# Performance work log

Hardware: AMD Instinct MI355X
Metric: run time of the kernel (lower is better)

The kernel has to match this reference:

```python
import jax, jax.numpy as jnp
import numpy as np

B, N, D = 2, 4096, 640      # batch, latent tokens, model dim
H, DH = 8, 80               # heads, head dim (H*DH == D)
CN, CD = 77, 768            # context tokens, context dim (CLIP)
FF = 4 * D                  # GEGLU inner dim = 2560
EPS = 1e-5


def _ln(x, w, b):
    m = jnp.mean(x, axis=-1, keepdims=True)
    v = jnp.mean(jnp.square(x - m), axis=-1, keepdims=True)
    return (x - m) * jax.lax.rsqrt(v + EPS) * w + b


def _attn(xq, xkv, wq, wk, wv, wo, bo):
    b, n, _ = xq.shape
    m = xkv.shape[1]
    q = (xq @ wq).reshape(b, n, H, DH).transpose(0, 2, 1, 3)   # b h n d
    k = (xkv @ wk).reshape(b, m, H, DH).transpose(0, 2, 1, 3)  # b h m d
    v = (xkv @ wv).reshape(b, m, H, DH).transpose(0, 2, 1, 3)
    scores = jnp.einsum('bhid,bhjd->bhij', q, k) * (DH ** -0.5)
    attn = jax.nn.softmax(scores, axis=-1)
    out = jnp.einsum('bhij,bhjd->bhid', attn, v)
    out = out.transpose(0, 2, 1, 3).reshape(b, n, H * DH)
    return out @ wo + bo


def setup_inputs() -> dict:
    key = jax.random.key(0)
    ks = jax.random.split(key, 20)
    s = 0.02
    r = lambda k, sh: (jax.random.normal(k, sh, jnp.float32) * s)
    return {
        'x': jax.random.normal(ks[0], (B, N, D), jnp.float32),
        'context': jax.random.normal(ks[1], (B, CN, CD), jnp.float32),
        'ln1_w': jnp.ones((D,), jnp.float32), 'ln1_b': jnp.zeros((D,), jnp.float32),
        'ln2_w': jnp.ones((D,), jnp.float32), 'ln2_b': jnp.zeros((D,), jnp.float32),
        'ln3_w': jnp.ones((D,), jnp.float32), 'ln3_b': jnp.zeros((D,), jnp.float32),
        'wq1': r(ks[2], (D, D)), 'wk1': r(ks[3], (D, D)), 'wv1': r(ks[4], (D, D)),
        'wo1': r(ks[5], (D, D)), 'bo1': jnp.zeros((D,), jnp.float32),
        'wq2': r(ks[6], (D, D)), 'wk2': r(ks[7], (CD, D)), 'wv2': r(ks[8], (CD, D)),
        'wo2': r(ks[9], (D, D)), 'bo2': jnp.zeros((D,), jnp.float32),
        'w_ff1': r(ks[10], (D, 2 * FF)), 'b_ff1': jnp.zeros((2 * FF,), jnp.float32),
        'w_ff2': r(ks[11], (FF, D)), 'b_ff2': jnp.zeros((D,), jnp.float32),
    }


def reference(x, context,
              ln1_w, ln1_b, ln2_w, ln2_b, ln3_w, ln3_b,
              wq1, wk1, wv1, wo1, bo1,
              wq2, wk2, wv2, wo2, bo2,
              w_ff1, b_ff1, w_ff2, b_ff2):
    # self-attention block
    h = _ln(x, ln1_w, ln1_b)
    x = _attn(h, h, wq1, wk1, wv1, wo1, bo1) + x
    # cross-attention block (k/v from context)
    h = _ln(x, ln2_w, ln2_b)
    x = _attn(h, context, wq2, wk2, wv2, wo2, bo2) + x
    # GEGLU feed-forward
    h = _ln(x, ln3_w, ln3_b)
    proj = h @ w_ff1 + b_ff1
    a, g = jnp.split(proj, 2, axis=-1)
    ff = (a * jax.nn.gelu(g, approximate=False)) @ w_ff2 + b_ff2
    return ff + x
```

## Files before the change

kernel.cpp:

```cpp
#include <hip/hip_runtime.h>
#include <hip/hip_bf16.h>

typedef __hip_bfloat16 bf16;
typedef short s16x8 __attribute__((ext_vector_type(8)));
typedef short s16x4 __attribute__((ext_vector_type(4)));
typedef float f32x4 __attribute__((ext_vector_type(4)));

#define SCALE_DH 0.11180339887498949f
#define QSCALE   0.16129820878f

static __device__ __forceinline__ float b2f(short u) {
  union { float f; unsigned int i; } x;
  x.i = ((unsigned int)(unsigned short)u) << 16;
  return x.f;
}

static __device__ __forceinline__ float tof(float x) { return x; }
static __device__ __forceinline__ float tof(bf16 x) { return __bfloat162float(x); }

static __device__ __forceinline__ void gload16(const bf16* g, bf16* l) {
  __builtin_amdgcn_global_load_lds((__attribute__((address_space(1))) const void*)g,
                                   (__attribute__((address_space(3))) void*)l, 16, 0, 0);
}

struct PrepArgs {
  const float* src[10];
  bf16* dst[10];
  int R[10], C[10], cb[10], base[10];
  int cvtbase;
  const float* ctx;
  bf16* ctxb;
};

__global__ __launch_bounds__(256) void prep_kernel(PrepArgs a) {
  const int bid = blockIdx.x;
  if (bid >= a.cvtbase) {
    const int n = 154 * 768;
    int i = ((bid - a.cvtbase) * 256 + threadIdx.x) * 4;
    if (i + 4 <= n) {
      float4 v = *(const float4*)(a.ctx + i);
      a.ctxb[i + 0] = __float2bfloat16(v.x);
      a.ctxb[i + 1] = __float2bfloat16(v.y);
      a.ctxb[i + 2] = __float2bfloat16(v.z);
      a.ctxb[i + 3] = __float2bfloat16(v.w);
    } else {
      for (int k = i; k < n; ++k) a.ctxb[k] = __float2bfloat16(a.ctx[k]);
    }
    return;
  }
  int jid = 0;
#pragma unroll
  for (int k = 1; k < 10; ++k)
    if (bid >= a.base[k]) jid = k;
  const float* in = a.src[jid];
  bf16* out = a.dst[jid];
  const int R = a.R[jid], C = a.C[jid];
  const int lb = bid - a.base[jid];
  const int cblk = lb % a.cb[jid], rblk = lb / a.cb[jid];
  __shared__ float t[32][33];
  const int tx = threadIdx.x & 31, ty = threadIdx.x >> 5;
  const long r0 = (long)rblk * 32, c0 = (long)cblk * 32;
#pragma unroll
  for (int i = 0; i < 4; ++i)
    t[ty + 8 * i][tx] = in[(r0 + ty + 8 * i) * C + c0 + tx];
  __syncthreads();
#pragma unroll
  for (int i = 0; i < 4; ++i)
    out[(c0 + ty + 8 * i) * R + r0 + tx] = __float2bfloat16(t[tx][ty + 8 * i]);
}

template <typename T>
__global__ __launch_bounds__(256) void ln_kernel(const T* __restrict__ x,
                                                 const float* __restrict__ w,
                                                 const float* __restrict__ b,
                                                 bf16* __restrict__ out) {
  const int wv = threadIdx.x >> 6, l = threadIdx.x & 63;
  const long row = (long)blockIdx.x * 4 + wv;
  const T* xr = x + row * 640;
  float v[10];
  float s = 0.f;
#pragma unroll
  for (int j = 0; j < 10; ++j) { v[j] = tof(xr[l + 64 * j]); s += v[j]; }
#pragma unroll
  for (int o = 32; o > 0; o >>= 1) s += __shfl_xor(s, o);
  const float mean = s * (1.f / 640.f);
  float vs = 0.f;
#pragma unroll
  for (int j = 0; j < 10; ++j) { float d = v[j] - mean; vs += d * d; }
#pragma unroll
  for (int o = 32; o > 0; o >>= 1) vs += __shfl_xor(vs, o);
  const float rstd = rsqrtf(vs * (1.f / 640.f) + 1e-5f);
  bf16* orow = out + row * 640;
#pragma unroll
  for (int j = 0; j < 10; ++j) {
    int d = l + 64 * j;
    orow[d] = __float2bfloat16((v[j] - mean) * rstd * w[d] + b[d]);
  }
}

template <int EPI>
__global__ __launch_bounds__(256) void gemm_kernel(const bf16* __restrict__ A,
                                                   const bf16* __restrict__ Bt,
                                                   const float* __restrict__ bias,
                                                   const float* __restrict__ res,
                                                   void* __restrict__ Cout,
                                                   int M, int K, int ldc) {
  __shared__ bf16 Ash[128 * 64];
  __shared__ bf16 Bsh[128 * 64];
  const int tid = threadIdx.x, w = tid >> 6, l = tid & 63;
  const int m0 = blockIdx.x * 128, n0 = blockIdx.y * 128;
  const int mb = (w >> 1) * 64, nb = (w & 1) * 64;
  const int lo = l & 15, lg = l >> 4, lo7 = l & 7;
  const f32x4 fz = {0.f, 0.f, 0.f, 0.f};
  f32x4 acc[4][4];
#pragma unroll
  for (int i = 0; i < 4; ++i)
#pragma unroll
    for (int j = 0; j < 4; ++j) acc[i][j] = fz;

  const int g = tid;
  const int gr = g >> 3;
  const int gcsw = 8 * ((g & 7) ^ (gr & 7));
  const bf16* pa[4];
  const bf16* pb[4];
  bf16* la[4];
  bf16* lb[4];
#pragma unroll
  for (int s = 0; s < 4; ++s) {
    const int rl = gr + 32 * s;
    int ra = m0 + rl; if (ra >= M) ra = M - 1;
    pa[s] = A + (long)ra * K + gcsw;
    pb[s] = Bt + (long)(n0 + rl) * K + gcsw;
    la[s] = Ash + (g + 256 * s) * 8;
    lb[s] = Bsh + (g + 256 * s) * 8;
  }

  for (int k0 = 0; k0 < K; k0 += 64) {
    __syncthreads();
#pragma unroll
    for (int s = 0; s < 4; ++s) {
      gload16(pa[s], la[s]); pa[s] += 64;
      gload16(pb[s], lb[s]); pb[s] += 64;
    }
    __syncthreads();
#pragma unroll
    for (int kk = 0; kk < 2; ++kk) {
      const int sl = ((kk * 4 + lg) ^ lo7) * 8;
      s16x8 a[4], b[4];
#pragma unroll
      for (int i = 0; i < 4; ++i)
        a[i] = *(const s16x8*)(Ash + (mb + i * 16 + lo) * 64 + sl);
#pragma unroll
      for (int j = 0; j < 4; ++j)
        b[j] = *(const s16x8*)(Bsh + (nb + j * 16 + lo) * 64 + sl);
#pragma unroll
      for (int i = 0; i < 4; ++i)
#pragma unroll
        for (int j = 0; j < 4; ++j)
          acc[i][j] = __builtin_amdgcn_mfma_f32_16x16x32_bf16(a[i], b[j], acc[i][j], 0, 0, 0);
    }
  }
  const int rb = m0 + mb + lg * 4;
  const int cb = n0 + nb + lo;
#pragma unroll
  for (int i = 0; i < 4; ++i) {
#pragma unroll
    for (int j = 0; j < 4; ++j) {
      const int col = cb + j * 16;
      if (EPI == 3 && col >= 1280) {
        const int t = col - 1280;
        const int hh = t / 80, dh = t % 80;
        const int row0 = rb + i * 16;
        const int bb = row0 >> 12, n = row0 & 4095;
        s16x4 pk;
#pragma unroll
        for (int r = 0; r < 4; ++r)
          pk[r] = (short)__bfloat16_as_ushort(__float2bfloat16(acc[i][j][r]));
        bf16* vt = (bf16*)res;
        *(s16x4*)(vt + (long)(bb * 8 + hh) * 327680 + (long)dh * 4096 + n) = pk;
        continue;
      }
#pragma unroll
      for (int r = 0; r < 4; ++r) {
        const int row = rb + i * 16 + r;
        if (row < M)
          ((bf16*)Cout)[(long)row * ldc + col] = __float2bfloat16(acc[i][j][r]);
      }
    }
  }
}

template <int EPI>
__global__ __launch_bounds__(256) void gemm64_kernel(const bf16* __restrict__ A,
                                                     const bf16* __restrict__ Bt,
                                                     const float* __restrict__ bias,
                                                     const void* __restrict__ res,
                                                     void* __restrict__ Cout,
                                                     int K, int ldc) {
  __shared__ bf16 Ash[64 * 64];
  __shared__ bf16 Bsh[128 * 64];
  const int tid = threadIdx.x, w = tid >> 6, l = tid & 63;
  const int m0 = blockIdx.x * 64, n0 = blockIdx.y * 128;
  const int mb = (w & 1) * 32, nb = (w >> 1) * 64;
  const int lo = l & 15, lg = l >> 4, lo7 = l & 7;
  const f32x4 fz = {0.f, 0.f, 0.f, 0.f};
  f32x4 acc[2][4];
#pragma unroll
  for (int i = 0; i < 2; ++i)
#pragma unroll
    for (int j = 0; j < 4; ++j) acc[i][j] = fz;

  const int g = tid;
  const int gr = g >> 3;
  const int gcsw = 8 * ((g & 7) ^ (gr & 7));
  const bf16* pa[2];
  const bf16* pb[4];
  bf16* la[2];
  bf16* lb[4];
#pragma unroll
  for (int s = 0; s < 2; ++s) {
    pa[s] = A + (long)(m0 + gr + 32 * s) * K + gcsw;
    la[s] = Ash + (g + 256 * s) * 8;
  }
#pragma unroll
  for (int s = 0; s < 4; ++s) {
    pb[s] = Bt + (long)(n0 + gr + 32 * s) * K + gcsw;
    lb[s] = Bsh + (g + 256 * s) * 8;
  }

  for (int k0 = 0; k0 < K; k0 += 64) {
    __syncthreads();
#pragma unroll
    for (int s = 0; s < 2; ++s) { gload16(pa[s], la[s]); pa[s] += 64; }
#pragma unroll
    for (int s = 0; s < 4; ++s) { gload16(pb[s], lb[s]); pb[s] += 64; }
    __syncthreads();
#pragma unroll
    for (int kk = 0; kk < 2; ++kk) {
      const int sl = ((kk * 4 + lg) ^ lo7) * 8;
      s16x8 a[2], b[4];
#pragma unroll
      for (int i = 0; i < 2; ++i)
        a[i] = *(const s16x8*)(Ash + (mb + i * 16 + lo) * 64 + sl);
#pragma unroll
      for (int j = 0; j < 4; ++j)
        b[j] = *(const s16x8*)(Bsh + (nb + j * 16 + lo) * 64 + sl);
#pragma unroll
      for (int i = 0; i < 2; ++i)
#pragma unroll
        for (int j = 0; j < 4; ++j)
          acc[i][j] = __builtin_amdgcn_mfma_f32_16x16x32_bf16(a[i], b[j], acc[i][j], 0, 0, 0);
    }
  }
  const int rb = m0 + mb + lg * 4;
  const int cb = n0 + nb + lo;
#pragma unroll
  for (int i = 0; i < 2; ++i) {
#pragma unroll
    for (int j = 0; j < 4; ++j) {
      const int col = cb + j * 16;
      float bv = 0.f;
      if (EPI >= 4) bv = bias[col];
#pragma unroll
      for (int r = 0; r < 4; ++r) {
        const int row = rb + i * 16 + r;
        const long idx = (long)row * ldc + col;
        float v = acc[i][j][r] + bv;
        if (EPI == 4) {
          v += ((const float*)res)[idx];
          ((bf16*)Cout)[idx] = __float2bfloat16(v);
        } else if (EPI == 5) {
          v += __bfloat162float(((const bf16*)res)[idx]);
          ((bf16*)Cout)[idx] = __float2bfloat16(v);
        } else if (EPI == 6) {
          v += __bfloat162float(((const bf16*)res)[idx]);
          ((float*)Cout)[idx] = v;
        } else {
          ((bf16*)Cout)[idx] = __float2bfloat16(v);
        }
      }
    }
  }
}

__global__ __launch_bounds__(256, 3) void flash_kernel(const bf16* __restrict__ qkv,
                                                       const bf16* __restrict__ vT,
                                                       bf16* __restrict__ out) {
  __shared__ bf16 Ksh[64 * 80];
  __shared__ bf16 Vsh[80 * 64];
  const int bh = blockIdx.y, b = bh >> 3, h = bh & 7;
  const int tid = threadIdx.x, w = tid >> 6, l = tid & 63;
  const int r0 = blockIdx.x * 128 + w * 32;
  const int lg = l >> 4, lo = l & 15, lo7 = l & 7;
  const int sb = l & 48;
  const s16x8 sz = {0, 0, 0, 0, 0, 0, 0, 0};
  const f32x4 fz = {0.f, 0.f, 0.f, 0.f};

  s16x8 qa[2][3];
#pragma unroll
  for (int gq = 0; gq < 2; ++gq) {
    const bf16* qp = qkv + (long)(b * 4096 + r0 + gq * 16 + lo) * 1920 + h * 80;
    qa[gq][0] = *(const s16x8*)(qp + lg * 8);
    qa[gq][1] = *(const s16x8*)(qp + 32 + lg * 8);
    qa[gq][2] = (lg < 2) ? *(const s16x8*)(qp + 64 + lg * 8) : sz;
#pragma unroll
    for (int f = 0; f < 3; ++f) {
      s16x8 q = qa[gq][f], r;
#pragma unroll
      for (int i = 0; i < 8; ++i)
        r[i] = (short)(__bfloat16_as_ushort(__float2bfloat16(b2f(q[i]) * QSCALE)));
      qa[gq][f] = r;
    }
  }

  const bf16* kp[3];
  const int nbatch = (w < 2) ? 3 : 2;
#pragma unroll
  for (int it = 0; it < 3; ++it) {
    int g = tid + 256 * it;
    int gc = (g < 640) ? g : 0;
    int krow = gc / 10, ksl = gc % 10;
    int ksrc = (ksl < 8) ? (ksl ^ (krow & 7)) : (8 + ((ksl - 8) ^ ((krow >> 2) & 1)));
    kp[it] = qkv + (long)(b * 4096 + krow) * 1920 + 640 + h * 80 + ksrc * 8;
  }
  const bf16* vp0 = vT + (long)bh * 327680 + (long)(tid >> 3) * 4096 +
                    (((tid & 7) ^ ((tid >> 3) & 7)) * 8);
  const int soff0 = tid * 8;

  const int voff0 = (((lg >> 1) + 0) ^ lo7) * 8 + 4 * (lg & 1);
  const int voff1 = (((lg >> 1) + 2) ^ lo7) * 8 + 4 * (lg & 1);
  const int voff2 = (((lg >> 1) + 4) ^ lo7) * 8 + 4 * (lg & 1);
  const int voff3 = (((lg >> 1) + 6) ^ lo7) * 8 + 4 * (lg & 1);

  float lrA = 0.f, lrB = 0.f;
  f32x4 oA[5], oB[5];
#pragma unroll
  for (int dt = 0; dt < 5; ++dt) { oA[dt] = fz; oB[dt] = fz; }

#pragma unroll
  for (int it = 0; it < 3; ++it) {
    if (it < nbatch) {
      gload16(kp[it], Ksh + soff0 + 2048 * it); kp[it] += 64 * 1920;
      gload16(vp0 + (long)it * 131072, Vsh + soff0 + 2048 * it);
    }
  }
  __syncthreads();

  for (int kt = 0; kt < 64; ++kt) {
    unsigned paA[8], paB[8];
    f32x4 s0A, s0B, s1A, s1B;
    {
      s16x8 kb0 = *(const s16x8*)(Ksh + lo * 80 + ((lg ^ lo7)) * 8);
      s16x8 kb1 = *(const s16x8*)(Ksh + lo * 80 + (((4 + lg) ^ lo7)) * 8);
      s16x8 kb2 = (lg < 2) ? *(const s16x8*)(Ksh + lo * 80 + 64 + ((lg ^ ((lo >> 2) & 1))) * 8) : sz;
      __builtin_amdgcn_s_setprio(1);
      s0A = __builtin_amdgcn_mfma_f32_16x16x32_bf16(kb0, qa[0][0], fz, 0, 0, 0);
      s0A = __builtin_amdgcn_mfma_f32_16x16x32_bf16(kb1, qa[0][1], s0A, 0, 0, 0);
      s0A = __builtin_amdgcn_mfma_f32_16x16x32_bf16(kb2, qa[0][2], s0A, 0, 0, 0);
      s0B = __builtin_amdgcn_mfma_f32_16x16x32_bf16(kb0, qa[1][0], fz, 0, 0, 0);
      s0B = __builtin_amdgcn_mfma_f32_16x16x32_bf16(kb1, qa[1][1], s0B, 0, 0, 0);
      s0B = __builtin_amdgcn_mfma_f32_16x16x32_bf16(kb2, qa[1][2], s0B, 0, 0, 0);
      __builtin_amdgcn_s_setprio(0);
    }
#pragma unroll
    for (int ntl = 1; ntl <= 4; ++ntl) {
      if (ntl < 4) {
        s16x8 kb0 = *(const s16x8*)(Ksh + (ntl * 16 + lo) * 80 + ((lg ^ lo7)) * 8);
        s16x8 kb1 = *(const s16x8*)(Ksh + (ntl * 16 + lo) * 80 + (((4 + lg) ^ lo7)) * 8);
        s16x8 kb2 = (lg < 2)
                        ? *(const s16x8*)(Ksh + (ntl * 16 + lo) * 80 + 64 + ((lg ^ ((lo >> 2) & 1))) * 8)
                        : sz;
        __builtin_amdgcn_s_setprio(1);
        s1A = __builtin_amdgcn_mfma_f32_16x16x32_bf16(kb0, qa[0][0], fz, 0, 0, 0);
        s1A = __builtin_amdgcn_mfma_f32_16x16x32_bf16(kb1, qa[0][1], s1A, 0, 0, 0);
        s1A = __builtin_amdgcn_mfma_f32_16x16x32_bf16(kb2, qa[0][2], s1A, 0, 0, 0);
        s1B = __builtin_amdgcn_mfma_f32_16x16x32_bf16(kb0, qa[1][0], fz, 0, 0, 0);
        s1B = __builtin_amdgcn_mfma_f32_16x16x32_bf16(kb1, qa[1][1], s1B, 0, 0, 0);
        s1B = __builtin_amdgcn_mfma_f32_16x16x32_bf16(kb2, qa[1][2], s1B, 0, 0, 0);
        __builtin_amdgcn_s_setprio(0);
      }
      {
        const int pidx = ntl - 1;
        float a0 = __builtin_amdgcn_exp2f(s0A[0]);
        float a1 = __builtin_amdgcn_exp2f(s0A[1]);
        float a2 = __builtin_amdgcn_exp2f(s0A[2]);
        float a3 = __builtin_amdgcn_exp2f(s0A[3]);
        lrA += (a0 + a1) + (a2 + a3);
        unsigned u0, u1;
        asm("v_cvt_pk_bf16_f32 %0, %1, %2" : "=v"(u0) : "v"(a0), "v"(a1));
        asm("v_cvt_pk_bf16_f32 %0, %1, %2" : "=v"(u1) : "v"(a2), "v"(a3));
        paA[pidx * 2] = u0;
        paA[pidx * 2 + 1] = u1;
        float b0 = __builtin_amdgcn_exp2f(s0B[0]);
        float b1 = __builtin_amdgcn_exp2f(s0B[1]);
        float b2 = __builtin_amdgcn_exp2f(s0B[2]);
        float b3 = __builtin_amdgcn_exp2f(s0B[3]);
        lrB += (b0 + b1) + (b2 + b3);
        asm("v_cvt_pk_bf16_f32 %0, %1, %2" : "=v"(u0) : "v"(b0), "v"(b1));
        asm("v_cvt_pk_bf16_f32 %0, %1, %2" : "=v"(u1) : "v"(b2), "v"(b3));
        paB[pidx * 2] = u0;
        paB[pidx * 2 + 1] = u1;
      }
      s0A = s1A;
      s0B = s1B;
    }

    typedef unsigned u32x2 __attribute__((ext_vector_type(2)));
    s16x8 frA0, frA1, frB0, frB1;
    {
      u32x2* p;
      p = (u32x2*)&frA0; p[0] = (u32x2){paA[0], paA[1]}; p[1] = (u32x2){paA[2], paA[3]};
      p = (u32x2*)&frA1; p[0] = (u32x2){paA[4], paA[5]}; p[1] = (u32x2){paA[6], paA[7]};
      p = (u32x2*)&frB0; p[0] = (u32x2){paB[0], paB[1]}; p[1] = (u32x2){paB[2], paB[3]};
      p = (u32x2*)&frB1; p[0] = (u32x2){paB[4], paB[5]}; p[1] = (u32x2){paB[6], paB[7]};
    }

    __syncthreads();

    if (kt < 63) {
#pragma unroll
      for (int it = 0; it < 3; ++it) {
        if (it < nbatch) { gload16(kp[it], Ksh + soff0 + 2048 * it); kp[it] += 64 * 1920; }
      }
    }

    __builtin_amdgcn_s_setprio(1);
#pragma unroll
    for (int dt = 0; dt < 5; ++dt) {
      const bf16* vrow = Vsh + (dt * 16 + lo) * 64;
      s16x4 w00 = *(const s16x4*)(vrow + voff0);
      s16x4 w01 = *(const s16x4*)(vrow + voff1);
      s16x4 w10 = *(const s16x4*)(vrow + voff2);
      s16x4 w11 = *(const s16x4*)(vrow + voff3);
      s16x8 vb0 = __builtin_shufflevector(w00, w01, 0, 1, 2, 3, 4, 5, 6, 7);
      s16x8 vb1 = __builtin_shufflevector(w10, w11, 0, 1, 2, 3, 4, 5, 6, 7);
      oA[dt] = __builtin_amdgcn_mfma_f32_16x16x32_bf16(frA0, vb0, oA[dt], 0, 0, 0);
      oA[dt] = __builtin_amdgcn_mfma_f32_16x16x32_bf16(frA1, vb1, oA[dt], 0, 0, 0);
      oB[dt] = __builtin_amdgcn_mfma_f32_16x16x32_bf16(frB0, vb0, oB[dt], 0, 0, 0);
      oB[dt] = __builtin_amdgcn_mfma_f32_16x16x32_bf16(frB1, vb1, oB[dt], 0, 0, 0);
    }
    __builtin_amdgcn_s_setprio(0);

    __syncthreads();

    if (kt < 63) {
#pragma unroll
      for (int it = 0; it < 3; ++it) {
        if (it < nbatch) gload16(vp0 + (long)(kt + 1) * 64 + (long)it * 131072,
                                 Vsh + soff0 + 2048 * it);
      }
    }
  }

  {
    float ssum = lrA;
    ssum += __shfl_xor(ssum, 16);
    ssum += __shfl_xor(ssum, 32);
    const float linv = 1.f / ssum;
    float li[4];
#pragma unroll
    for (int r = 0; r < 4; ++r) li[r] = __shfl(linv, sb + lg * 4 + r);
    bf16* ob = out + (long)(b * 4096 + r0 + lg * 4) * 640 + h * 80 + lo;
#pragma unroll
    for (int r = 0; r < 4; ++r)
#pragma unroll
      for (int dt = 0; dt < 5; ++dt)
        ob[(long)r * 640 + dt * 16] = __float2bfloat16(oA[dt][r] * li[r]);
  }
  {
    float ssum = lrB;
    ssum += __shfl_xor(ssum, 16);
    ssum += __shfl_xor(ssum, 32);
    const float linv = 1.f / ssum;
    float li[4];
#pragma unroll
    for (int r = 0; r < 4; ++r) li[r] = __shfl(linv, sb + lg * 4 + r);
    bf16* ob = out + (long)(b * 4096 + r0 + 16 + lg * 4) * 640 + h * 80 + lo;
#pragma unroll
    for (int r = 0; r < 4; ++r)
#pragma unroll
      for (int dt = 0; dt < 5; ++dt)
        ob[(long)r * 640 + dt * 16] = __float2bfloat16(oB[dt][r] * li[r]);
  }
}

__global__ __launch_bounds__(256) void cross_kernel(const bf16* __restrict__ q2,
                                                    const bf16* __restrict__ kv2,
                                                    bf16* __restrict__ out) {
  __shared__ bf16 Ksh2[80 * 88];
  __shared__ bf16 Vsh2[80 * 88];
  const int bh = blockIdx.y, b = bh >> 3, h = bh & 7;
  const int tid = threadIdx.x, w = tid >> 6, l = tid & 63;
  const int r0 = blockIdx.x * 128 + w * 32;
  const int lg = l >> 4, lo = l & 15;
  const int sb = l & 48;
  const s16x8 sz = {0, 0, 0, 0, 0, 0, 0, 0};
  const f32x4 fz = {0.f, 0.f, 0.f, 0.f};

  s16x8 qa[2][3];
#pragma unroll
  for (int gq = 0; gq < 2; ++gq) {
    const bf16* qp = q2 + (long)(b * 4096 + r0 + gq * 16 + lo) * 640 + h * 80;
    qa[gq][0] = *(const s16x8*)(qp + lg * 8);
    qa[gq][1] = *(const s16x8*)(qp + 32 + lg * 8);
    qa[gq][2] = (lg < 2) ? *(const s16x8*)(qp + 64 + lg * 8) : sz;
#pragma unroll
    for (int f = 0; f < 3; ++f) {
      s16x8 q = qa[gq][f], r;
#pragma unroll
      for (int i = 0; i < 8; ++i)
        r[i] = (short)(__bfloat16_as_ushort(__float2bfloat16(b2f(q[i]) * QSCALE)));
      qa[gq][f] = r;
    }
  }

  for (int c = tid; c < 800; c += 256) {
    int row = c / 10, s = c % 10;
    s16x8 v = sz;
    if (row < 77)
      v = *(const s16x8*)(kv2 + (long)(b * 77 + row) * 1280 + h * 80 + s * 8);
    *(s16x8*)(Ksh2 + row * 88 + s * 8) = v;
  }
  for (int c = tid; c < 770; c += 256) {
    int j = c / 10, d8 = (c % 10) * 8;
    s16x8 v = *(const s16x8*)(kv2 + (long)(b * 77 + j) * 1280 + 640 + h * 80 + d8);
    const short* vs = (const short*)&v;
#pragma unroll
    for (int i = 0; i < 8; ++i) ((short*)Vsh2)[(d8 + i) * 88 + j] = vs[i];
  }
  if (tid < 240) {
    int d = tid / 3, j = 77 + tid % 3;
    ((short*)Vsh2)[d * 88 + j] = 0;
  }
  __syncthreads();

  float lrA = 0.f, lrB = 0.f;
  f32x4 oA[5], oB[5];
#pragma unroll
  for (int dt = 0; dt < 5; ++dt) { oA[dt] = fz; oB[dt] = fz; }

  unsigned paA[10], paB[10];
  f32x4 s0A, s0B, s1A, s1B;
  {
    s16x8 kb0 = *(const s16x8*)(Ksh2 + lo * 88 + lg * 8);
    s16x8 kb1 = *(const s16x8*)(Ksh2 + lo * 88 + 32 + lg * 8);
    s16x8 kb2 = (lg < 2) ? *(const s16x8*)(Ksh2 + lo * 88 + 64 + lg * 8) : sz;
    __builtin_amdgcn_s_setprio(1);
    s0A = __builtin_amdgcn_mfma_f32_16x16x32_bf16(kb0, qa[0][0], fz, 0, 0, 0);
    s0A = __builtin_amdgcn_mfma_f32_16x16x32_bf16(kb1, qa[0][1], s0A, 0, 0, 0);
    s0A = __builtin_amdgcn_mfma_f32_16x16x32_bf16(kb2, qa[0][2], s0A, 0, 0, 0);
    s0B = __builtin_amdgcn_mfma_f32_16x16x32_bf16(kb0, qa[1][0], fz, 0, 0, 0);
    s0B = __builtin_amdgcn_mfma_f32_16x16x32_bf16(kb1, qa[1][1], s0B, 0, 0, 0);
    s0B = __builtin_amdgcn_mfma_f32_16x16x32_bf16(kb2, qa[1][2], s0B, 0, 0, 0);
    __builtin_amdgcn_s_setprio(0);
  }
#pragma unroll
  for (int ntl = 1; ntl <= 5; ++ntl) {
    if (ntl < 5) {
      s16x8 kb0 = *(const s16x8*)(Ksh2 + (ntl * 16 + lo) * 88 + lg * 8);
      s16x8 kb1 = *(const s16x8*)(Ksh2 + (ntl * 16 + lo) * 88 + 32 + lg * 8);
      s16x8 kb2 = (lg < 2) ? *(const s16x8*)(Ksh2 + (ntl * 16 + lo) * 88 + 64 + lg * 8) : sz;
      __builtin_amdgcn_s_setprio(1);
      s1A = __builtin_amdgcn_mfma_f32_16x16x32_bf16(kb0, qa[0][0], fz, 0, 0, 0);
      s1A = __builtin_amdgcn_mfma_f32_16x16x32_bf16(kb1, qa[0][1], s1A, 0, 0, 0);
      s1A = __builtin_amdgcn_mfma_f32_16x16x32_bf16(kb2, qa[0][2], s1A, 0, 0, 0);
      s1B = __builtin_amdgcn_mfma_f32_16x16x32_bf16(kb0, qa[1][0], fz, 0, 0, 0);
      s1B = __builtin_amdgcn_mfma_f32_16x16x32_bf16(kb1, qa[1][1], s1B, 0, 0, 0);
      s1B = __builtin_amdgcn_mfma_f32_16x16x32_bf16(kb2, qa[1][2], s1B, 0, 0, 0);
      __builtin_amdgcn_s_setprio(0);
    }
    {
      const int pidx = ntl - 1;
      float a0 = __builtin_amdgcn_exp2f(s0A[0]);
      float a1 = __builtin_amdgcn_exp2f(s0A[1]);
      float a2 = __builtin_amdgcn_exp2f(s0A[2]);
      float a3 = __builtin_amdgcn_exp2f(s0A[3]);
      float b0 = __builtin_amdgcn_exp2f(s0B[0]);
      float b1 = __builtin_amdgcn_exp2f(s0B[1]);
      float b2 = __builtin_amdgcn_exp2f(s0B[2]);
      float b3 = __builtin_amdgcn_exp2f(s0B[3]);
      if (pidx == 4) {
        if (lg * 4 + 1 >= 13) { a1 = 0.f; b1 = 0.f; }
        if (lg * 4 + 2 >= 13) { a2 = 0.f; b2 = 0.f; }
        if (lg * 4 + 3 >= 13) { a3 = 0.f; b3 = 0.f; }
      }
      lrA += (a0 + a1) + (a2 + a3);
      lrB += (b0 + b1) + (b2 + b3);
      unsigned u0, u1;
      asm("v_cvt_pk_bf16_f32 %0, %1, %2" : "=v"(u0) : "v"(a0), "v"(a1));
      asm("v_cvt_pk_bf16_f32 %0, %1, %2" : "=v"(u1) : "v"(a2), "v"(a3));
      paA[pidx * 2] = u0;
      paA[pidx * 2 + 1] = u1;
      asm("v_cvt_pk_bf16_f32 %0, %1, %2" : "=v"(u0) : "v"(b0), "v"(b1));
      asm("v_cvt_pk_bf16_f32 %0, %1, %2" : "=v"(u1) : "v"(b2), "v"(b3));
      paB[pidx * 2] = u0;
      paB[pidx * 2 + 1] = u1;
    }
    s0A = s1A;
    s0B = s1B;
  }

  typedef unsigned u32x2 __attribute__((ext_vector_type(2)));
  s16x8 frA0, frA1, frA2, frB0, frB1, frB2;
  {
    u32x2* p;
    p = (u32x2*)&frA0; p[0] = (u32x2){paA[0], paA[1]}; p[1] = (u32x2){paA[2], paA[3]};
    p = (u32x2*)&frA1; p[0] = (u32x2){paA[4], paA[5]}; p[1] = (u32x2){paA[6], paA[7]};
    p = (u32x2*)&frA2; p[0] = (u32x2){paA[8], paA[9]}; p[1] = (u32x2){0u, 0u};
    p = (u32x2*)&frB0; p[0] = (u32x2){paB[0], paB[1]}; p[1] = (u32x2){paB[2], paB[3]};
    p = (u32x2*)&frB1; p[0] = (u32x2){paB[4], paB[5]}; p[1] = (u32x2){paB[6], paB[7]};
    p = (u32x2*)&frB2; p[0] = (u32x2){paB[8], paB[9]}; p[1] = (u32x2){0u, 0u};
  }

  __builtin_amdgcn_s_setprio(1);
#pragma unroll
  for (int dt = 0; dt < 5; ++dt) {
    const bf16* vrow = Vsh2 + (dt * 16 + lo) * 88;
    s16x4 w00 = *(const s16x4*)(vrow + 4 * lg);
    s16x4 w01 = *(const s16x4*)(vrow + 16 + 4 * lg);
    s16x4 w10 = *(const s16x4*)(vrow + 32 + 4 * lg);
    s16x4 w11 = *(const s16x4*)(vrow + 48 + 4 * lg);
    s16x4 w20 = *(const s16x4*)(vrow + 64 + 4 * lg);
    s16x8 vb0 = __builtin_shufflevector(w00, w01, 0, 1, 2, 3, 4, 5, 6, 7);
    s16x8 vb1 = __builtin_shufflevector(w10, w11, 0, 1, 2, 3, 4, 5, 6, 7);
    s16x8 vb2 = __builtin_shufflevector(w20, w20, 0, 1, 2, 3, 0, 1, 2, 3);
    oA[dt] = __builtin_amdgcn_mfma_f32_16x16x32_bf16(frA0, vb0, oA[dt], 0, 0, 0);
    oA[dt] = __builtin_amdgcn_mfma_f32_16x16x32_bf16(frA1, vb1, oA[dt], 0, 0, 0);
    oA[dt] = __builtin_amdgcn_mfma_f32_16x16x32_bf16(frA2, vb2, oA[dt], 0, 0, 0);
    oB[dt] = __builtin_amdgcn_mfma_f32_16x16x32_bf16(frB0, vb0, oB[dt], 0, 0, 0);
    oB[dt] = __builtin_amdgcn_mfma_f32_16x16x32_bf16(frB1, vb1, oB[dt], 0, 0, 0);
    oB[dt] = __builtin_amdgcn_mfma_f32_16x16x32_bf16(frB2, vb2, oB[dt], 0, 0, 0);
  }
  __builtin_amdgcn_s_setprio(0);

  {
    float ssum = lrA;
    ssum += __shfl_xor(ssum, 16);
    ssum += __shfl_xor(ssum, 32);
    const float linv = 1.f / ssum;
    float li[4];
#pragma unroll
    for (int r = 0; r < 4; ++r) li[r] = __shfl(linv, sb + lg * 4 + r);
    bf16* ob = out + (long)(b * 4096 + r0 + lg * 4) * 640 + h * 80 + lo;
#pragma unroll
    for (int r = 0; r < 4; ++r)
#pragma unroll
      for (int dt = 0; dt < 5; ++dt)
        ob[(long)r * 640 + dt * 16] = __float2bfloat16(oA[dt][r] * li[r]);
  }
  {
    float ssum = lrB;
    ssum += __shfl_xor(ssum, 16);
    ssum += __shfl_xor(ssum, 32);
    const float linv = 1.f / ssum;
    float li[4];
#pragma unroll
    for (int r = 0; r < 4; ++r) li[r] = __shfl(linv, sb + lg * 4 + r);
    bf16* ob = out + (long)(b * 4096 + r0 + 16 + lg * 4) * 640 + h * 80 + lo;
#pragma unroll
    for (int r = 0; r < 4; ++r)
#pragma unroll
      for (int dt = 0; dt < 5; ++dt)
        ob[(long)r * 640 + dt * 16] = __float2bfloat16(oB[dt][r] * li[r]);
  }
}

__global__ __launch_bounds__(256) void geglu_kernel(const bf16* __restrict__ A,
                                                    const bf16* __restrict__ Bt,
                                                    const float* __restrict__ bias,
                                                    bf16* __restrict__ Cout) {
  __shared__ bf16 Ash[128 * 64];
  __shared__ bf16 Bsh[2][64 * 64];
  const int tid = threadIdx.x, w = tid >> 6, l = tid & 63;
  const int m0 = blockIdx.x * 128, n0 = blockIdx.y * 64;
  const int lo = l & 15, lg = l >> 4, lo7 = l & 7;
  const int mb = w * 32;
  const f32x4 fz = {0.f, 0.f, 0.f, 0.f};
  f32x4 accA[2][4], accG[2][4];
#pragma unroll
  for (int i = 0; i < 2; ++i)
#pragma unroll
    for (int j = 0; j < 4; ++j) { accA[i][j] = fz; accG[i][j] = fz; }

  const int g = tid;
  const int gr = g >> 3;
  const int gcsw = 8 * ((g & 7) ^ (gr & 7));
  const bf16* pa[4];
  const bf16* pb[2][2];
  bf16* la[4];
  bf16* lb[2][2];
#pragma unroll
  for (int s = 0; s < 4; ++s) {
    pa[s] = A + (long)(m0 + gr + 32 * s) * 640 + gcsw;
    la[s] = Ash + (g + 256 * s) * 8;
  }
#pragma unroll
  for (int q = 0; q < 2; ++q)
#pragma unroll
    for (int s = 0; s < 2; ++s) {
      pb[q][s] = Bt + (long)(n0 + q * 2560 + gr + 32 * s) * 640 + gcsw;
      lb[q][s] = Bsh[q] + (g + 256 * s) * 8;
    }

  for (int k0 = 0; k0 < 640; k0 += 64) {
    __syncthreads();
#pragma unroll
    for (int s = 0; s < 4; ++s) { gload16(pa[s], la[s]); pa[s] += 64; }
#pragma unroll
    for (int q = 0; q < 2; ++q)
#pragma unroll
      for (int s = 0; s < 2; ++s) { gload16(pb[q][s], lb[q][s]); pb[q][s] += 64; }
    __syncthreads();
#pragma unroll
    for (int kk = 0; kk < 2; ++kk) {
      const int sl = ((kk * 4 + lg) ^ lo7) * 8;
      s16x8 a[2], ba[4], bg[4];
#pragma unroll
      for (int i = 0; i < 2; ++i)
        a[i] = *(const s16x8*)(Ash + (mb + i * 16 + lo) * 64 + sl);
#pragma unroll
      for (int j = 0; j < 4; ++j) {
        ba[j] = *(const s16x8*)(Bsh[0] + (j * 16 + lo) * 64 + sl);
        bg[j] = *(const s16x8*)(Bsh[1] + (j * 16 + lo) * 64 + sl);
      }
#pragma unroll
      for (int i = 0; i < 2; ++i)
#pragma unroll
        for (int j = 0; j < 4; ++j) {
          accA[i][j] = __builtin_amdgcn_mfma_f32_16x16x32_bf16(a[i], ba[j], accA[i][j], 0, 0, 0);
          accG[i][j] = __builtin_amdgcn_mfma_f32_16x16x32_bf16(a[i], bg[j], accG[i][j], 0, 0, 0);
        }
    }
  }
#pragma unroll
  for (int i = 0; i < 2; ++i) {
#pragma unroll
    for (int j = 0; j < 4; ++j) {
      const int col = n0 + j * 16 + lo;
      const float bA = bias[col];
      const float bG = bias[2560 + col];
#pragma unroll
      for (int r = 0; r < 4; ++r) {
        const long row = m0 + mb + i * 16 + lg * 4 + r;
        const float av = accA[i][j][r] + bA;
        const float gv = accG[i][j][r] + bG;
        const float ge = 0.5f * gv * (1.f + erff(gv * 0.70710678118654752f));
        Cout[row * 2560 + col] = __float2bfloat16(av * ge);
      }
    }
  }
}

extern "C" void kernel_launch(void* const* d_in, const int* in_sizes, int n_in,
                              void* d_out, int out_size, void* d_ws, size_t ws_size,
                              hipStream_t stream) {
  (void)in_sizes; (void)n_in; (void)out_size; (void)ws_size;
  const float* x    = (const float*)d_in[0];
  const float* ctx  = (const float*)d_in[1];
  const float* ln1w = (const float*)d_in[2];
  const float* ln1b = (const float*)d_in[3];
  const float* ln2w = (const float*)d_in[4];
  const float* ln2b = (const float*)d_in[5];
  const float* ln3w = (const float*)d_in[6];
  const float* ln3b = (const float*)d_in[7];
  const float* wq1  = (const float*)d_in[8];
  const float* wk1  = (const float*)d_in[9];
  const float* wv1  = (const float*)d_in[10];
  const float* wo1  = (const float*)d_in[11];
  const float* bo1  = (const float*)d_in[12];
  const float* wq2  = (const float*)d_in[13];
  const float* wk2  = (const float*)d_in[14];
  const float* wv2  = (const float*)d_in[15];
  const float* wo2  = (const float*)d_in[16];
  const float* bo2  = (const float*)d_in[17];
  const float* wff1 = (const float*)d_in[18];
  const float* bff1 = (const float*)d_in[19];
  const float* wff2 = (const float*)d_in[20];
  const float* bff2 = (const float*)d_in[21];

  char* ws = (char*)d_ws;
  bf16* Wqkv1 = (bf16*)(ws + 0);
  bf16* Wo1t  = (bf16*)(ws + 2457600);
  bf16* Wq2t  = (bf16*)(ws + 3276800);
  bf16* Wkv2t = (bf16*)(ws + 4096000);
  bf16* Wo2t  = (bf16*)(ws + 6062080);
  bf16* Wff1t = (bf16*)(ws + 6881280);
  bf16* Wff2t = (bf16*)(ws + 13434880);
  bf16* Ctxb  = (bf16*)(ws + 16711680);
  bf16* Hln   = (bf16*)(ws + 16948224);
  bf16* X2b   = (bf16*)(ws + 27433984);
  bf16* X3b   = (bf16*)(ws + 48405504);
  bf16* Qkv   = (bf16*)(ws + 69377024);
  bf16* Ffin  = Qkv;
  bf16* Vt    = (bf16*)(ws + 100834304);
  bf16* Ao    = (bf16*)(ws + 111320064);
  bf16* Q2    = (bf16*)(ws + 121805824);
  bf16* Kv2   = (bf16*)(ws + 132291584);
  float* Outf = (float*)d_out;

  dim3 blk(256);

  PrepArgs pa;
  const float* srcs[10] = {wq1, wk1, wv1, wo1, wq2, wk2, wv2, wo2, wff1, wff2};
  bf16* dsts[10] = {Wqkv1, Wqkv1 + 640 * 640, Wqkv1 + 2 * 640 * 640, Wo1t, Wq2t,
                    Wkv2t, Wkv2t + 640 * 768, Wo2t, Wff1t, Wff2t};
  int Rs[10] = {640, 640, 640, 640, 640, 768, 768, 640, 640, 2560};
  int Cs[10] = {640, 640, 640, 640, 640, 640, 640, 640, 5120, 640};
  int baseacc = 0;
  for (int j = 0; j < 10; ++j) {
    pa.src[j] = srcs[j];
    pa.dst[j] = dsts[j];
    pa.R[j] = Rs[j];
    pa.C[j] = Cs[j];
    pa.cb[j] = Cs[j] / 32;
    pa.base[j] = baseacc;
    baseacc += (Cs[j] / 32) * (Rs[j] / 32);
  }
  pa.cvtbase = baseacc;
  pa.ctx = ctx;
  pa.ctxb = Ctxb;
  const int prep_blocks = baseacc + 116;
  prep_kernel<<<prep_blocks, blk, 0, stream>>>(pa);

  ln_kernel<float><<<2048, blk, 0, stream>>>(x, ln1w, ln1b, Hln);
  gemm_kernel<3><<<dim3(64, 15), blk, 0, stream>>>(Hln, Wqkv1, nullptr, (const float*)Vt, Qkv, 8192, 640, 1920);
  flash_kernel<<<dim3(32, 16), blk, 0, stream>>>(Qkv, Vt, Ao);
  gemm64_kernel<4><<<dim3(128, 5), blk, 0, stream>>>(Ao, Wo1t, bo1, x, X2b, 640, 640);
  ln_kernel<bf16><<<2048, blk, 0, stream>>>(X2b, ln2w, ln2b, Hln);
  gemm64_kernel<0><<<dim3(128, 5), blk, 0, stream>>>(Hln, Wq2t, nullptr, nullptr, Q2, 640, 640);
  gemm_kernel<0><<<dim3(2, 10), blk, 0, stream>>>(Ctxb, Wkv2t, nullptr, nullptr, Kv2, 154, 768, 1280);
  cross_kernel<<<dim3(32, 16), blk, 0, stream>>>(Q2, Kv2, Ao);
  gemm64_kernel<5><<<dim3(128, 5), blk, 0, stream>>>(Ao, Wo2t, bo2, X2b, X3b, 640, 640);
  ln_kernel<bf16><<<2048, blk, 0, stream>>>(X3b, ln3w, ln3b, Hln);
  geglu_kernel<<<dim3(64, 40), blk, 0, stream>>>(Hln, Wff1t, bff1, Ffin);
  gemm64_kernel<6><<<dim3(128, 5), blk, 0, stream>>>(Ffin, Wff2t, bff2, X3b, Outf, 2560, 640);
}
```

Baseline: 345.0 us.

## Double-buffer K/V shared tiles in flash attention kernel

Splits the K and V LDS tiles into two buffers and issues the global-to-LDS loads for the next key tile at the start of each iteration, while the current buffer is being used. One of the two per-iteration barriers goes away, and the load latency can overlap with the QK^T, softmax and PV MFMA work. LDS use per block doubles from about 20KB to 40KB, which may hurt occupancy at the 3-blocks-per-CU launch bound. Correctness relies on the global_load_lds completing before the single trailing barrier, which needs a proper vmcnt wait.

```diff
diff --git a/kernel.cpp b/kernel.cpp
--- a/kernel.cpp
+++ b/kernel.cpp
@@ -286,8 +286,8 @@
 __global__ __launch_bounds__(256, 3) void flash_kernel(const bf16* __restrict__ qkv,
                                                        const bf16* __restrict__ vT,
                                                        bf16* __restrict__ out) {
-  __shared__ bf16 Ksh[64 * 80];
-  __shared__ bf16 Vsh[80 * 64];
+  __shared__ bf16 Ksh[2][64 * 80];
+  __shared__ bf16 Vsh[2][80 * 64];
   const int bh = blockIdx.y, b = bh >> 3, h = bh & 7;
   const int tid = threadIdx.x, w = tid >> 6, l = tid & 63;
   const int r0 = blockIdx.x * 128 + w * 32;
@@ -340,19 +340,33 @@
 #pragma unroll
   for (int it = 0; it < 3; ++it) {
     if (it < nbatch) {
-      gload16(kp[it], Ksh + soff0 + 2048 * it); kp[it] += 64 * 1920;
-      gload16(vp0 + (long)it * 131072, Vsh + soff0 + 2048 * it);
+      gload16(kp[it], Ksh[0] + soff0 + 2048 * it); kp[it] += 64 * 1920;
+      gload16(vp0 + (long)it * 131072, Vsh[0] + soff0 + 2048 * it);
     }
   }
   __syncthreads();
 
   for (int kt = 0; kt < 64; ++kt) {
+    const int cur = kt & 1;
+    const bf16* kbuf = Ksh[cur];
+    const bf16* vbuf = Vsh[cur];
+
+    if (kt < 63) {
+#pragma unroll
+      for (int it = 0; it < 3; ++it) {
+        if (it < nbatch) {
+          gload16(kp[it], Ksh[cur ^ 1] + soff0 + 2048 * it); kp[it] += 64 * 1920;
+          gload16(vp0 + (long)(kt + 1) * 64 + (long)it * 131072, Vsh[cur ^ 1] + soff0 + 2048 * it);
+        }
+      }
+    }
+
     unsigned paA[8], paB[8];
     f32x4 s0A, s0B, s1A, s1B;
     {
-      s16x8 kb0 = *(const s16x8*)(Ksh + lo * 80 + ((lg ^ lo7)) * 8);
-      s16x8 kb1 = *(const s16x8*)(Ksh + lo * 80 + (((4 + lg) ^ lo7)) * 8);
-      s16x8 kb2 = (lg < 2) ? *(const s16x8*)(Ksh + lo * 80 + 64 + ((lg ^ ((lo >> 2) & 1))) * 8) : sz;
+      s16x8 kb0 = *(const s16x8*)(kbuf + lo * 80 + ((lg ^ lo7)) * 8);
+      s16x8 kb1 = *(const s16x8*)(kbuf + lo * 80 + (((4 + lg) ^ lo7)) * 8);
+      s16x8 kb2 = (lg < 2) ? *(const s16x8*)(kbuf + lo * 80 + 64 + ((lg ^ ((lo >> 2) & 1))) * 8) : sz;
       __builtin_amdgcn_s_setprio(1);
       s0A = __builtin_amdgcn_mfma_f32_16x16x32_bf16(kb0, qa[0][0], fz, 0, 0, 0);
       s0A = __builtin_amdgcn_mfma_f32_16x16x32_bf16(kb1, qa[0][1], s0A, 0, 0, 0);
@@ -365,10 +379,10 @@
 #pragma unroll
     for (int ntl = 1; ntl <= 4; ++ntl) {
       if (ntl < 4) {
-        s16x8 kb0 = *(const s16x8*)(Ksh + (ntl * 16 + lo) * 80 + ((lg ^ lo7)) * 8);
-        s16x8 kb1 = *(const s16x8*)(Ksh + (ntl * 16 + lo) * 80 + (((4 + lg) ^ lo7)) * 8);
+        s16x8 kb0 = *(const s16x8*)(kbuf + (ntl * 16 + lo) * 80 + ((lg ^ lo7)) * 8);
+        s16x8 kb1 = *(const s16x8*)(kbuf + (ntl * 16 + lo) * 80 + (((4 + lg) ^ lo7)) * 8);
         s16x8 kb2 = (lg < 2)
-                        ? *(const s16x8*)(Ksh + (ntl * 16 + lo) * 80 + 64 + ((lg ^ ((lo >> 2) & 1))) * 8)
+                        ? *(const s16x8*)(kbuf + (ntl * 16 + lo) * 80 + 64 + ((lg ^ ((lo >> 2) & 1))) * 8)
                         : sz;
         __builtin_amdgcn_s_setprio(1);
         s1A = __builtin_amdgcn_mfma_f32_16x16x32_bf16(kb0, qa[0][0], fz, 0, 0, 0);
@@ -415,19 +429,10 @@
       p = (u32x2*)&frB1; p[0] = (u32x2){paB[4], paB[5]}; p[1] = (u32x2){paB[6], paB[7]};
     }
 
-    __syncthreads();
-
-    if (kt < 63) {
-#pragma unroll
-      for (int it = 0; it < 3; ++it) {
-        if (it < nbatch) { gload16(kp[it], Ksh + soff0 + 2048 * it); kp[it] += 64 * 1920; }
-      }
-    }
-
     __builtin_amdgcn_s_setprio(1);
 #pragma unroll
     for (int dt = 0; dt < 5; ++dt) {
-      const bf16* vrow = Vsh + (dt * 16 + lo) * 64;
+      const bf16* vrow = vbuf + (dt * 16 + lo) * 64;
       s16x4 w00 = *(const s16x4*)(vrow + voff0);
       s16x4 w01 = *(const s16x4*)(vrow + voff1);
       s16x4 w10 = *(const s16x4*)(vrow + voff2);
@@ -442,14 +447,6 @@
     __builtin_amdgcn_s_setprio(0);
 
     __syncthreads();
-
-    if (kt < 63) {
-#pragma unroll
-      for (int it = 0; it < 3; ++it) {
-        if (it < nbatch) gload16(vp0 + (long)(kt + 1) * 64 + (long)it * 131072,
-                                 Vsh + soff0 + 2048 * it);
-      }
-    }
   }
 
   {
```

Result: no change. 343.7 us (-0.4%).
